# Kernel optimization log

Hardware: AMD Instinct MI355X
Metric: run time of the kernel (lower is better)

## Reference

```python
import jax, jax.numpy as jnp
import numpy as np

N = 200_000   # nodes in batched graph
E = 6_400_000 # edges
G = 1024      # graphs in the batch
H = 256       # hidden_dim


def setup_inputs() -> dict:
    key = jax.random.key(0)
    ks = jax.random.split(key, 20)
    src = jax.random.randint(ks[0], (E,), 0, N, dtype=jnp.int32)
    dst = jax.random.randint(ks[1], (E,), 0, N, dtype=jnp.int32)
    graph_ids = jnp.sort(jax.random.randint(ks[2], (N,), 0, G, dtype=jnp.int32))

    def lin(k, fi, fo):
        kw, kb = jax.random.split(k)
        s = 1.0 / np.sqrt(fi)
        return (jax.random.normal(kw, (fi, fo), jnp.float32) * s,
                jax.random.normal(kb, (fo,), jnp.float32) * s)

    W1, b1 = lin(ks[3], 4, H)
    W2, b2 = lin(ks[4], H, H)
    W3, b3 = lin(ks[5], H, H)
    W4, b4 = lin(ks[6], H, H)
    W5, b5 = lin(ks[7], H, H)
    Wl1, bl1 = lin(ks[8], H, H // 2)
    Wl2, bl2 = lin(ks[9], H // 2, 1)
    return dict(src=src, dst=dst, graph_ids=graph_ids,
                W1=W1, b1=b1, W2=W2, b2=b2, W3=W3, b3=b3, W4=W4, b4=b4,
                W5=W5, b5=b5, Wl1=Wl1, bl1=bl1, Wl2=Wl2, bl2=bl2)


def reference(src, dst, graph_ids, W1, b1, W2, b2, W3, b3, W4, b4, W5, b5,
              Wl1, bl1, Wl2, bl2):
    ones_e = jnp.ones((E,), jnp.float32)
    deg_in = jax.ops.segment_sum(ones_e, dst, num_segments=N)   # in_degrees
    deg_out = jax.ops.segment_sum(ones_e, src, num_segments=N)  # out_degrees

    # node features from in-degrees (as in the torch forward)
    h1 = deg_in
    h2 = (deg_in - 3.0 > 0).astype(jnp.float32)
    h3 = 3.0 / h1
    h4 = (deg_in - 4.0 > 0).astype(jnp.float32)
    h_ = jnp.stack([h1, h2, h3, h4], axis=1)  # [N,4]

    # DGL GraphConv norm='both': D_out^{-1/2} on src side, D_in^{-1/2} on dst side
    norm_src = jax.lax.rsqrt(jnp.clip(deg_out, 1.0))[:, None]  # [N,1]
    norm_dst = jax.lax.rsqrt(jnp.clip(deg_in, 1.0))[:, None]

    def gconv(x, W, b):
        xs = x * norm_src
        agg = jax.ops.segment_sum(xs[src], dst, num_segments=N)  # SpMM
        return (agg * norm_dst) @ W + b

    h = jnp.tanh(gconv(h_, W1, b1))
    h = jnp.tanh(gconv(h, W2, b2))
    h = jnp.tanh(gconv(h, W3, b3))
    h = jnp.tanh(gconv(h, W4, b4))
    h = jnp.tanh(gconv(h, W5, b5))  # [N,H]

    # dgl.mean_nodes: per-graph mean over nodes
    gsum = jax.ops.segment_sum(h, graph_ids, num_segments=G)           # [G,H]
    cnt = jax.ops.segment_sum(jnp.ones((N,), jnp.float32), graph_ids,
                              num_segments=G)[:, None]
    graph_emb = jnp.where(cnt > 0, gsum / jnp.clip(cnt, 1.0), 0.0)

    h_emb = jax.nn.leaky_relu(graph_emb @ Wl1 + bl1, negative_slope=0.01)
    # dropout is identity in eval mode
    pred = jax.nn.sigmoid(h_emb @ Wl2 + bl2)
    return pred, graph_emb, h
```

## Files before the change

kernel.cpp:

```cpp
#include <hip/hip_runtime.h>
#include <hip/hip_fp16.h>

#define NN 200000
#define EE 6400000
#define GG 1024
#define HH 256
#define RR 8
#define NB 782
#define NC 782
#define CHUNK 8192
#define CAP 9216

typedef _Float16 half8 __attribute__((ext_vector_type(8)));
typedef float floatx4 __attribute__((ext_vector_type(4)));
typedef unsigned int uintx2 __attribute__((ext_vector_type(2)));

__device__ __forceinline__ float fast_tanh(float x) {
  float e = __expf(2.0f * x);
  return 1.0f - 2.0f / (e + 1.0f);
}

__global__ void degree_src_kernel(const int* __restrict__ src, int* __restrict__ doutR) {
  int e = blockIdx.x * blockDim.x + threadIdx.x;
  if (e >= EE) return;
  atomicAdd(&doutR[(e & (RR - 1)) * NN + src[e]], 1);
}

__global__ void gptr_kernel(const int* __restrict__ gid, int* __restrict__ g_ptr) {
  int n = blockIdx.x * blockDim.x + threadIdx.x;
  if (n >= NN) return;
  int g = gid[n];
  int gp = (n == 0) ? -1 : gid[n - 1];
  for (int x = gp + 1; x <= g; ++x) g_ptr[x] = n;
  if (n == NN - 1) {
    for (int x = g + 1; x <= GG; ++x) g_ptr[x] = NN;
  }
}

__global__ __launch_bounds__(256) void hist1_kernel(const int* __restrict__ dst,
                                                    int* __restrict__ hist_t) {
  __shared__ int h[NB];
  int c = blockIdx.x, t = threadIdx.x;
  for (int b = t; b < NB; b += 256) h[b] = 0;
  __syncthreads();
  int e0 = c * CHUNK, e1 = min(e0 + CHUNK, EE);
  for (int e = e0 + t; e < e1; e += 256) atomicAdd(&h[dst[e] >> 8], 1);
  __syncthreads();
  for (int b = t; b < NB; b += 256) hist_t[b * NC + c] = h[b];
}

__global__ __launch_bounds__(256) void scanA4_kernel(int* __restrict__ a, int n,
                                                     int* __restrict__ bsum) {
  __shared__ int ws4[4];
  int t = threadIdx.x;
  int base = blockIdx.x * 1024 + t * 4;
  int v0 = 0, v1 = 0, v2 = 0, v3 = 0;
  if (base + 3 < n) {
    int4 q = *(const int4*)(a + base);
    v0 = q.x; v1 = q.y; v2 = q.z; v3 = q.w;
  } else {
    if (base + 0 < n) v0 = a[base + 0];
    if (base + 1 < n) v1 = a[base + 1];
    if (base + 2 < n) v2 = a[base + 2];
    if (base + 3 < n) v3 = a[base + 3];
  }
  int s = v0 + v1 + v2 + v3;
  int lane = t & 63, w = t >> 6;
  int x = s;
  for (int off = 1; off < 64; off <<= 1) {
    int y = __shfl_up(x, off);
    if (lane >= off) x += y;
  }
  if (lane == 63) ws4[w] = x;
  __syncthreads();
  if (t == 0) {
    int acc = 0;
    for (int k = 0; k < 4; ++k) { int tmp = ws4[k]; ws4[k] = acc; acc += tmp; }
  }
  __syncthreads();
  int e = ws4[w] + x - s;
  int o0 = e, o1 = e + v0, o2 = o1 + v1, o3 = o2 + v2;
  if (base + 3 < n) {
    int4 q; q.x = o0; q.y = o1; q.z = o2; q.w = o3;
    *(int4*)(a + base) = q;
  } else {
    if (base + 0 < n) a[base + 0] = o0;
    if (base + 1 < n) a[base + 1] = o1;
    if (base + 2 < n) a[base + 2] = o2;
    if (base + 3 < n) a[base + 3] = o3;
  }
  if (t == 255) bsum[blockIdx.x] = ws4[3] + x;
}

__global__ __launch_bounds__(1024) void scanB_kernel(const int* __restrict__ bsum, int nb,
                                                     int* __restrict__ boffs) {
  __shared__ int wsum[16];
  int t = threadIdx.x;
  int lane = t & 63, w = t >> 6;
  int v = (t < nb) ? bsum[t] : 0;
  int x = v;
  for (int off = 1; off < 64; off <<= 1) {
    int y = __shfl_up(x, off);
    if (lane >= off) x += y;
  }
  if (lane == 63) wsum[w] = x;
  __syncthreads();
  if (t < 16) {
    int s = wsum[t];
    for (int off = 1; off < 16; off <<= 1) {
      int y = __shfl_up(s, off);
      if (t >= off) s += y;
    }
    wsum[t] = s;
  }
  __syncthreads();
  int waveoff = (w > 0) ? wsum[w - 1] : 0;
  int excl = waveoff + (x - v);
  if (t <= nb) boffs[t] = excl;
}

__global__ void addC4_kernel(int* __restrict__ a, int n, const int* __restrict__ boffs) {
  int i = blockIdx.x * blockDim.x + threadIdx.x;
  if (i < n) a[i] += boffs[i >> 10];
}

__global__ void bucketptr_kernel(const int* __restrict__ hist_t, int* __restrict__ bucket_ptr) {
  int b = blockIdx.x * blockDim.x + threadIdx.x;
  if (b < NB) bucket_ptr[b] = hist_t[b * NC];
  if (b == NB) bucket_ptr[NB] = EE;
}

__global__ __launch_bounds__(256) void scatter1_kernel(const int* __restrict__ src,
                                                       const int* __restrict__ dst,
                                                       const int* __restrict__ hist_t,
                                                       uint2* __restrict__ pairs) {
  __shared__ int cur[NB];
  int c = blockIdx.x, t = threadIdx.x;
  for (int b = t; b < NB; b += 256) cur[b] = hist_t[b * NC + c];
  __syncthreads();
  int e0 = c * CHUNK, e1 = min(e0 + CHUNK, EE);
  for (int e = e0 + t; e < e1; e += 256) {
    int d = dst[e], s = src[e];
    int pos = atomicAdd(&cur[d >> 8], 1);
    uint2 p; p.x = (unsigned)d; p.y = (unsigned)s;
    pairs[pos] = p;
  }
}

__global__ __launch_bounds__(256) void bucket_kernel(const uint2* __restrict__ pairs,
                                                     const int* __restrict__ bucket_ptr,
                                                     int* __restrict__ col,
                                                     int* __restrict__ row_ptr) {
  __shared__ int rhist[256];
  __shared__ int rcur[256];
  __shared__ int ws4[4];
  __shared__ int stage[CAP];
  int b = blockIdx.x, t = threadIdx.x;
  int row0 = b << 8;
  int p0 = bucket_ptr[b], p1 = bucket_ptr[b + 1];
  int cnt = p1 - p0;
  rhist[t] = 0;
  __syncthreads();
  for (int i = t; i < cnt; i += 256) {
    int d = (int)pairs[p0 + i].x;
    atomicAdd(&rhist[d & 255], 1);
  }
  __syncthreads();
  int v = rhist[t];
  int lane = t & 63, w = t >> 6;
  int x = v;
  for (int off = 1; off < 64; off <<= 1) {
    int y = __shfl_up(x, off);
    if (lane >= off) x += y;
  }
  if (lane == 63) ws4[w] = x;
  __syncthreads();
  if (t == 0) {
    int acc = 0;
    for (int k = 0; k < 4; ++k) { int tmp = ws4[k]; ws4[k] = acc; acc += tmp; }
  }
  __syncthreads();
  int excl = ws4[w] + x - v;
  rcur[t] = excl;
  int row = row0 + t;
  if (row < NN) row_ptr[row] = p0 + excl;
  if (b == NB - 1 && t == 0) row_ptr[NN] = EE;
  __syncthreads();
  for (int i = t; i < cnt; i += 256) {
    uint2 p = pairs[p0 + i];
    int pos = atomicAdd(&rcur[(int)p.x & 255], 1);
    if (pos < CAP) stage[pos] = (int)p.y;
    else col[p0 + pos] = (int)p.y;
  }
  __syncthreads();
  int lim = min(cnt, CAP);
  for (int i = t; i < lim; i += 256) col[p0 + i] = stage[i];
}

__global__ void feature_kernel(const int* __restrict__ row_ptr, const int* __restrict__ doutR,
                               float* __restrict__ norm_src, float* __restrict__ norm_dst,
                               float4* __restrict__ xs1) {
  int n = blockIdx.x * blockDim.x + threadIdx.x;
  if (n >= NN) return;
  int dii = row_ptr[n + 1] - row_ptr[n];
  int doo = 0;
#pragma unroll
  for (int r = 0; r < RR; ++r) doo += doutR[r * NN + n];
  float di = (float)dii;
  float dofl = (float)doo;
  float ns = rsqrtf(fmaxf(dofl, 1.0f));
  float nd = rsqrtf(fmaxf(di, 1.0f));
  norm_src[n] = ns;
  norm_dst[n] = nd;
  float h1 = di;
  float h2 = (di - 3.0f > 0.0f) ? 1.0f : 0.0f;
  float h3 = 3.0f / di;
  float h4 = (di - 4.0f > 0.0f) ? 1.0f : 0.0f;
  float4 o;
  o.x = h1 * ns; o.y = h2 * ns; o.z = h3 * ns; o.w = h4 * ns;
  xs1[n] = o;
}

__global__ void spmm4_kernel(const int* __restrict__ rp, const int* __restrict__ col,
                             const float4* __restrict__ xs1, const float* __restrict__ norm_dst,
                             float4* __restrict__ agg4) {
  int n = blockIdx.x * blockDim.x + threadIdx.x;
  if (n >= NN) return;
  int e0 = rp[n], e1 = rp[n + 1];
  float ax = 0.f, ay = 0.f, az = 0.f, aw = 0.f;
  for (int e = e0; e < e1; ++e) {
    int s = __builtin_nontemporal_load(&col[e]);
    float4 v = xs1[s];
    ax += v.x; ay += v.y; az += v.z; aw += v.w;
  }
  float nd = norm_dst[n];
  float4 o; o.x = ax * nd; o.y = ay * nd; o.z = az * nd; o.w = aw * nd;
  agg4[n] = o;
}

__device__ __forceinline__ void acc_row(uint2 v, float& a0, float& a1, float& a2, float& a3) {
  __half2 h0 = *reinterpret_cast<__half2*>(&v.x);
  __half2 h1 = *reinterpret_cast<__half2*>(&v.y);
  float2 f0 = __half22float2(h0);
  float2 f1 = __half22float2(h1);
  a0 += f0.x; a1 += f0.y; a2 += f1.x; a3 += f1.y;
}

__global__ __launch_bounds__(256) void spmm256_kernel(
    const int* __restrict__ rp, const int* __restrict__ col,
    const __half* __restrict__ hs, const float* __restrict__ norm_dst,
    __half* __restrict__ aggH) {
  int wid = (blockIdx.x * blockDim.x + threadIdx.x) >> 6;
  int lane = threadIdx.x & 63;
  if (wid >= NN) return;
  int e0 = rp[wid], e1 = rp[wid + 1];
  float a0 = 0.f, a1 = 0.f, a2 = 0.f, a3 = 0.f;
  const __half* hp = hs + lane * 4;
  int e = e0;
  for (; e + 16 <= e1; e += 16) {
    int s[16];
#pragma unroll
    for (int u = 0; u < 16; ++u)
      s[u] = __builtin_amdgcn_readfirstlane(__builtin_nontemporal_load(&col[e + u]));
    uint2 v[16];
#pragma unroll
    for (int u = 0; u < 16; ++u) v[u] = *(const uint2*)(hp + (size_t)s[u] * HH);
#pragma unroll
    for (int u = 0; u < 16; ++u) acc_row(v[u], a0, a1, a2, a3);
  }
  for (; e + 4 <= e1; e += 4) {
    int s[4];
#pragma unroll
    for (int u = 0; u < 4; ++u)
      s[u] = __builtin_amdgcn_readfirstlane(__builtin_nontemporal_load(&col[e + u]));
    uint2 v[4];
#pragma unroll
    for (int u = 0; u < 4; ++u) v[u] = *(const uint2*)(hp + (size_t)s[u] * HH);
#pragma unroll
    for (int u = 0; u < 4; ++u) acc_row(v[u], a0, a1, a2, a3);
  }
  for (; e < e1; ++e) {
    int s = __builtin_amdgcn_readfirstlane(__builtin_nontemporal_load(&col[e]));
    uint2 v = *(const uint2*)(hp + (size_t)s * HH);
    acc_row(v, a0, a1, a2, a3);
  }
  float nd = norm_dst[wid];
  __half2 p0 = __floats2half2_rn(a0 * nd, a1 * nd);
  __half2 p1 = __floats2half2_rn(a2 * nd, a3 * nd);
  uintx2 o;
  o[0] = *(unsigned*)&p0;
  o[1] = *(unsigned*)&p1;
  __builtin_nontemporal_store(o, (uintx2*)(aggH + (size_t)wid * HH + lane * 4));
}

__global__ __launch_bounds__(256) void transform4_kernel(
    const float* __restrict__ agg, const float* __restrict__ W, const float* __restrict__ b,
    const float* __restrict__ norm_src, __half* __restrict__ hs_out) {
  __shared__ float tile[64 * 4];
  int t = threadIdx.x;
  int rowbase = blockIdx.x * 64;
  const float4* srcp = (const float4*)(agg + (size_t)rowbase * 4);
  float4* dst4 = (float4*)tile;
  for (int i = t; i < 64; i += 256) dst4[i] = srcp[i];
  __syncthreads();
  int w = t >> 6, lane = t & 63;
  int c0 = lane * 4;
  float acc[16][4];
#pragma unroll
  for (int r = 0; r < 16; ++r) {
    acc[r][0] = 0.f; acc[r][1] = 0.f; acc[r][2] = 0.f; acc[r][3] = 0.f;
  }
  const float* tw = tile + (size_t)(w * 16) * 4;
#pragma unroll
  for (int k = 0; k < 4; ++k) {
    float4 wv = *(const float4*)(W + (size_t)k * HH + c0);
#pragma unroll
    for (int r = 0; r < 16; ++r) {
      float a = tw[r * 4 + k];
      acc[r][0] += a * wv.x;
      acc[r][1] += a * wv.y;
      acc[r][2] += a * wv.z;
      acc[r][3] += a * wv.w;
    }
  }
  float4 bv = *(const float4*)(b + c0);
#pragma unroll
  for (int r = 0; r < 16; ++r) {
    int row = rowbase + w * 16 + r;
    float ns = norm_src[row];
    float y0 = fast_tanh(acc[r][0] + bv.x) * ns;
    float y1 = fast_tanh(acc[r][1] + bv.y) * ns;
    float y2 = fast_tanh(acc[r][2] + bv.z) * ns;
    float y3 = fast_tanh(acc[r][3] + bv.w) * ns;
    __half2 p0 = __floats2half2_rn(y0, y1);
    __half2 p1 = __floats2half2_rn(y2, y3);
    uint2 o = make_uint2(*(unsigned*)&p0, *(unsigned*)&p1);
    *(uint2*)(hs_out + (size_t)row * HH + c0) = o;
  }
}

__global__ void repack_w_kernel(const float* __restrict__ W2, const float* __restrict__ W3,
                                const float* __restrict__ W4, const float* __restrict__ W5,
                                __half* __restrict__ Wf) {
  int t = blockIdx.x * blockDim.x + threadIdx.x;
  int which = t >> 16;
  int u = t & 65535;
  const float* W = (which == 0) ? W2 : (which == 1) ? W3 : (which == 2) ? W4 : W5;
  int b = u & 7;
  int lane = (u >> 3) & 63;
  int tile = (u >> 9) & 15;
  int ks = u >> 13;
  int k = ks * 32 + (lane >> 4) * 8 + b;
  int c = tile * 16 + (lane & 15);
  Wf[t] = __float2half(W[k * HH + c]);
}

__global__ __launch_bounds__(256) void gemm_mfma_kernel(
    const __half* __restrict__ aggH, const __half* __restrict__ Wf,
    const float* __restrict__ bias, const float* __restrict__ norm_src,
    __half* __restrict__ hs_out, float* h_out) {
  int w = threadIdx.x >> 6;
  int lane = threadIdx.x & 63;
  int l15 = lane & 15, l4 = lane >> 4;
  int row0 = blockIdx.x * 64;
  floatx4 acc[4][4];
#pragma unroll
  for (int m = 0; m < 4; ++m)
#pragma unroll
    for (int n = 0; n < 4; ++n) acc[m][n] = (floatx4)(0.0f);

#pragma unroll
  for (int ks = 0; ks < 8; ++ks) {
    int k0 = ks * 32 + l4 * 8;
    half8 af[4];
#pragma unroll
    for (int m = 0; m < 4; ++m)
      af[m] = *(const half8*)(aggH + (size_t)(row0 + m * 16 + l15) * HH + k0);
    half8 bf[4];
#pragma unroll
    for (int n = 0; n < 4; ++n)
      bf[n] = *(const half8*)(Wf + ((size_t)(ks * 16 + w * 4 + n) * 64 + lane) * 8);
#pragma unroll
    for (int m = 0; m < 4; ++m)
#pragma unroll
      for (int n = 0; n < 4; ++n)
        acc[m][n] = __builtin_amdgcn_mfma_f32_16x16x32_f16(af[m], bf[n], acc[m][n], 0, 0, 0);
  }

  float ns[16];
  if (!h_out) {
#pragma unroll
    for (int m = 0; m < 4; ++m)
#pragma unroll
      for (int r = 0; r < 4; ++r) ns[m * 4 + r] = norm_src[row0 + m * 16 + l4 * 4 + r];
  }
#pragma unroll
  for (int n = 0; n < 4; ++n) {
    int c = w * 64 + n * 16 + l15;
    float bb = bias[c];
#pragma unroll
    for (int m = 0; m < 4; ++m) {
#pragma unroll
      for (int r = 0; r < 4; ++r) {
        int row = row0 + m * 16 + l4 * 4 + r;
        float y = fast_tanh(acc[m][n][r] + bb);
        if (h_out) {
          h_out[(size_t)row * HH + c] = y;
        } else {
          hs_out[(size_t)row * HH + c] = (__half)(y * ns[m * 4 + r]);
        }
      }
    }
  }
}

__global__ void mean_kernel(const float* __restrict__ h, const int* __restrict__ g_ptr,
                            float* __restrict__ emb) {
  int g = blockIdx.x;
  int j = threadIdx.x;
  int s = g_ptr[g], e = g_ptr[g + 1];
  float sum = 0.f;
  for (int n = s; n < e; ++n) sum += h[(size_t)n * HH + j];
  int cnt = e - s;
  emb[(size_t)g * HH + j] = (cnt > 0) ? sum / (float)cnt : 0.0f;
}

__global__ __launch_bounds__(128) void mlp_kernel(const float* __restrict__ emb,
                                                  const float* __restrict__ Wl1,
                                                  const float* __restrict__ bl1,
                                                  const float* __restrict__ Wl2,
                                                  const float* __restrict__ bl2,
                                                  float* __restrict__ pred) {
  __shared__ float se[256];
  __shared__ float sh[128];
  int g = blockIdx.x, t = threadIdx.x;
  se[t] = emb[(size_t)g * HH + t];
  se[t + 128] = emb[(size_t)g * HH + t + 128];
  __syncthreads();
  float acc = bl1[t];
  for (int k = 0; k < 256; ++k) acc += se[k] * Wl1[k * 128 + t];
  float he = (acc > 0.f) ? acc : 0.01f * acc;
  sh[t] = he * Wl2[t];
  __syncthreads();
  if (t < 64) sh[t] += sh[t + 64];
  __syncthreads();
  if (t < 64) {
    float v = sh[t];
    for (int off = 32; off > 0; off >>= 1) v += __shfl_down(v, off);
    if (t == 0) {
      float z = v + bl2[0];
      pred[g] = 1.0f / (1.0f + expf(-z));
    }
  }
}

extern "C" void kernel_launch(void* const* d_in, const int* in_sizes, int n_in,
                              void* d_out, int out_size, void* d_ws, size_t ws_size,
                              hipStream_t stream) {
  const int* src = (const int*)d_in[0];
  const int* dst = (const int*)d_in[1];
  const int* gid = (const int*)d_in[2];
  const float* W1 = (const float*)d_in[3];
  const float* b1 = (const float*)d_in[4];
  const float* W2 = (const float*)d_in[5];
  const float* b2 = (const float*)d_in[6];
  const float* W3 = (const float*)d_in[7];
  const float* b3 = (const float*)d_in[8];
  const float* W4 = (const float*)d_in[9];
  const float* b4 = (const float*)d_in[10];
  const float* W5 = (const float*)d_in[11];
  const float* b5 = (const float*)d_in[12];
  const float* Wl1 = (const float*)d_in[13];
  const float* bl1 = (const float*)d_in[14];
  const float* Wl2 = (const float*)d_in[15];
  const float* bl2 = (const float*)d_in[16];

  char* ws = (char*)d_ws;
  size_t off = 0;
  auto alloc = [&](size_t bytes) -> void* {
    void* p = ws + off;
    off += (bytes + 255) & ~(size_t)255;
    return p;
  };

  int* col = (int*)alloc((size_t)EE * 4);
  int* row_ptr = (int*)alloc((size_t)(NN + 1) * 4);
  int* hist_t = (int*)alloc((size_t)NB * NC * 4);
  int* bucket_ptr = (int*)alloc((size_t)(NB + 1) * 4);
  int* bsum = (int*)alloc(1024 * 4);
  int* boffs = (int*)alloc(1025 * 4);
  int* g_ptr = (int*)alloc((size_t)(GG + 1) * 4);
  float* norm_src = (float*)alloc((size_t)NN * 4);
  float* norm_dst = (float*)alloc((size_t)NN * 4);
  float4* xs1 = (float4*)alloc((size_t)NN * 16);
  float4* agg4 = (float4*)alloc((size_t)NN * 16);
  __half* Wf = (__half*)alloc((size_t)4 * HH * HH * 2);
  int* doutR = (int*)alloc((size_t)RR * NN * 4);
  void* unionp = alloc((size_t)NN * HH * 2);
  uint2* pairs = (uint2*)unionp;
  __half* aggH = (__half*)unionp;

  float* outp = (float*)d_out;
  float* pred = outp;
  float* emb = outp + GG;
  float* hreg = outp + GG + (size_t)GG * HH;
  __half* hs = (__half*)hreg;

  hipMemsetAsync(doutR, 0, (size_t)RR * NN * 4, stream);

  degree_src_kernel<<<(EE + 255) / 256, 256, 0, stream>>>(src, doutR);
  gptr_kernel<<<(NN + 255) / 256, 256, 0, stream>>>(gid, g_ptr);
  repack_w_kernel<<<1024, 256, 0, stream>>>(W2, W3, W4, W5, Wf);

  const int nscan = NB * NC;
  const int nbA = (nscan + 1023) / 1024;
  hist1_kernel<<<NC, 256, 0, stream>>>(dst, hist_t);
  scanA4_kernel<<<nbA, 256, 0, stream>>>(hist_t, nscan, bsum);
  scanB_kernel<<<1, 1024, 0, stream>>>(bsum, nbA, boffs);
  addC4_kernel<<<(nscan + 255) / 256, 256, 0, stream>>>(hist_t, nscan, boffs);
  bucketptr_kernel<<<(NB + 256) / 256, 256, 0, stream>>>(hist_t, bucket_ptr);
  scatter1_kernel<<<NC, 256, 0, stream>>>(src, dst, hist_t, pairs);
  bucket_kernel<<<NB, 256, 0, stream>>>(pairs, bucket_ptr, col, row_ptr);

  feature_kernel<<<(NN + 255) / 256, 256, 0, stream>>>(row_ptr, doutR, norm_src, norm_dst, xs1);

  spmm4_kernel<<<(NN + 255) / 256, 256, 0, stream>>>(row_ptr, col, xs1, norm_dst, agg4);
  transform4_kernel<<<NN / 64, 256, 0, stream>>>((const float*)agg4, W1, b1, norm_src, hs);

  const float* bs[4] = {b2, b3, b4, b5};
  for (int l = 0; l < 4; ++l) {
    spmm256_kernel<<<NN / 4, 256, 0, stream>>>(row_ptr, col, hs, norm_dst, aggH);
    gemm_mfma_kernel<<<NN / 64, 256, 0, stream>>>(
        aggH, Wf + (size_t)l * HH * HH, bs[l], norm_src,
        hs, (l == 3) ? hreg : (float*)nullptr);
  }

  mean_kernel<<<GG, 256, 0, stream>>>(hreg, g_ptr, emb);
  mlp_kernel<<<GG, 128, 0, stream>>>(emb, Wl1, bl1, Wl2, bl2, pred);
}
```

Before: 2.961 ms.

## Split 256-wide SpMM into two 128-column passes for cache locality

Replaces the single SpMM over all 256 fp16 feature columns with two launches that each gather and accumulate one 128-column half. The intent is to shrink the randomly gathered working set per pass so more of it stays cache-resident. In exchange the column index and row pointer arrays are read twice, and each lane issues narrower 4-byte loads instead of 8-byte loads.

Measured after the change: 3.013 ms. Within noise of the previous version (+1.8%).

```diff
diff --git a/kernel.cpp b/kernel.cpp
--- a/kernel.cpp
+++ b/kernel.cpp
@@ -13,7 +13,6 @@
 
 typedef _Float16 half8 __attribute__((ext_vector_type(8)));
 typedef float floatx4 __attribute__((ext_vector_type(4)));
-typedef unsigned int uintx2 __attribute__((ext_vector_type(2)));
 
 __device__ __forceinline__ float fast_tanh(float x) {
   float e = __expf(2.0f * x);
@@ -238,59 +237,54 @@
   agg4[n] = o;
 }
 
-__device__ __forceinline__ void acc_row(uint2 v, float& a0, float& a1, float& a2, float& a3) {
-  __half2 h0 = *reinterpret_cast<__half2*>(&v.x);
-  __half2 h1 = *reinterpret_cast<__half2*>(&v.y);
-  float2 f0 = __half22float2(h0);
-  float2 f1 = __half22float2(h1);
-  a0 += f0.x; a1 += f0.y; a2 += f1.x; a3 += f1.y;
-}
-
-__global__ __launch_bounds__(256) void spmm256_kernel(
+__device__ __forceinline__ void acc_half2(unsigned v, float& a0, float& a1) {
+  __half2 h = *reinterpret_cast<__half2*>(&v);
+  float2 f = __half22float2(h);
+  a0 += f.x; a1 += f.y;
+}
+
+__global__ __launch_bounds__(256) void spmm128_kernel(
     const int* __restrict__ rp, const int* __restrict__ col,
     const __half* __restrict__ hs, const float* __restrict__ norm_dst,
-    __half* __restrict__ aggH) {
+    __half* __restrict__ aggH, int half) {
   int wid = (blockIdx.x * blockDim.x + threadIdx.x) >> 6;
   int lane = threadIdx.x & 63;
   if (wid >= NN) return;
   int e0 = rp[wid], e1 = rp[wid + 1];
-  float a0 = 0.f, a1 = 0.f, a2 = 0.f, a3 = 0.f;
-  const __half* hp = hs + lane * 4;
+  float a0 = 0.f, a1 = 0.f;
+  const __half* hp = hs + half * 128 + lane * 2;
   int e = e0;
   for (; e + 16 <= e1; e += 16) {
     int s[16];
 #pragma unroll
     for (int u = 0; u < 16; ++u)
       s[u] = __builtin_amdgcn_readfirstlane(__builtin_nontemporal_load(&col[e + u]));
-    uint2 v[16];
-#pragma unroll
-    for (int u = 0; u < 16; ++u) v[u] = *(const uint2*)(hp + (size_t)s[u] * HH);
-#pragma unroll
-    for (int u = 0; u < 16; ++u) acc_row(v[u], a0, a1, a2, a3);
+    unsigned v[16];
+#pragma unroll
+    for (int u = 0; u < 16; ++u) v[u] = *(const unsigned*)(hp + (size_t)s[u] * HH);
+#pragma unroll
+    for (int u = 0; u < 16; ++u) acc_half2(v[u], a0, a1);
   }
   for (; e + 4 <= e1; e += 4) {
     int s[4];
 #pragma unroll
     for (int u = 0; u < 4; ++u)
       s[u] = __builtin_amdgcn_readfirstlane(__builtin_nontemporal_load(&col[e + u]));
-    uint2 v[4];
-#pragma unroll
-    for (int u = 0; u < 4; ++u) v[u] = *(const uint2*)(hp + (size_t)s[u] * HH);
-#pragma unroll
-    for (int u = 0; u < 4; ++u) acc_row(v[u], a0, a1, a2, a3);
+    unsigned v[4];
+#pragma unroll
+    for (int u = 0; u < 4; ++u) v[u] = *(const unsigned*)(hp + (size_t)s[u] * HH);
+#pragma unroll
+    for (int u = 0; u < 4; ++u) acc_half2(v[u], a0, a1);
   }
   for (; e < e1; ++e) {
     int s = __builtin_amdgcn_readfirstlane(__builtin_nontemporal_load(&col[e]));
-    uint2 v = *(const uint2*)(hp + (size_t)s * HH);
-    acc_row(v, a0, a1, a2, a3);
+    unsigned v = *(const unsigned*)(hp + (size_t)s * HH);
+    acc_half2(v, a0, a1);
   }
   float nd = norm_dst[wid];
-  __half2 p0 = __floats2half2_rn(a0 * nd, a1 * nd);
-  __half2 p1 = __floats2half2_rn(a2 * nd, a3 * nd);
-  uintx2 o;
-  o[0] = *(unsigned*)&p0;
-  o[1] = *(unsigned*)&p1;
-  __builtin_nontemporal_store(o, (uintx2*)(aggH + (size_t)wid * HH + lane * 4));
+  __half2 p = __floats2half2_rn(a0 * nd, a1 * nd);
+  __builtin_nontemporal_store(*(unsigned*)&p,
+                              (unsigned*)(aggH + (size_t)wid * HH + half * 128 + lane * 2));
 }
 
 __global__ __launch_bounds__(256) void transform4_kernel(
@@ -529,7 +523,8 @@
 
   const float* bs[4] = {b2, b3, b4, b5};
   for (int l = 0; l < 4; ++l) {
-    spmm256_kernel<<<NN / 4, 256, 0, stream>>>(row_ptr, col, hs, norm_dst, aggH);
+    spmm128_kernel<<<NN / 4, 256, 0, stream>>>(row_ptr, col, hs, norm_dst, aggH, 0);
+    spmm128_kernel<<<NN / 4, 256, 0, stream>>>(row_ptr, col, hs, norm_dst, aggH, 1);
     gemm_mfma_kernel<<<NN / 64, 256, 0, stream>>>(
         aggH, Wf + (size_t)l * HH * HH, bs[l], norm_src,
         hs, (l == 3) ? hreg : (float*)nullptr);
```

## Fuse SpMM aggregation with MFMA GEMM and compute out-degree via bucket sort

Applied to the files above, without the earlier changes.

Replaces the separate spmm256 and gemm kernels for layers 2-4 with one fused kernel. It aggregates 64 rows into an LDS tile and runs the MFMA transform from there, so the fp16 aggregate buffer no longer makes a round trip through global memory. It also replaces the atomic global out-degree histogram (8 replicated counters plus a memset) with a radix-style scatter of src and a per-bucket shared-memory histogram. The trade-offs are lower occupancy, since each block serializes 16 rows per wave of gather before the GEMM, and extra scan and scatter passes for the degree computation.

After: 2.969 ms. No clear change (+0.3%).

```diff
diff --git a/kernel.cpp b/kernel.cpp
--- a/kernel.cpp
+++ b/kernel.cpp
@@ -5,11 +5,11 @@
 #define EE 6400000
 #define GG 1024
 #define HH 256
-#define RR 8
 #define NB 782
 #define NC 782
 #define CHUNK 8192
 #define CAP 9216
+#define LP 264
 
 typedef _Float16 half8 __attribute__((ext_vector_type(8)));
 typedef float floatx4 __attribute__((ext_vector_type(4)));
@@ -18,12 +18,6 @@
 __device__ __forceinline__ float fast_tanh(float x) {
   float e = __expf(2.0f * x);
   return 1.0f - 2.0f / (e + 1.0f);
-}
-
-__global__ void degree_src_kernel(const int* __restrict__ src, int* __restrict__ doutR) {
-  int e = blockIdx.x * blockDim.x + threadIdx.x;
-  if (e >= EE) return;
-  atomicAdd(&doutR[(e & (RR - 1)) * NN + src[e]], 1);
 }
 
 __global__ void gptr_kernel(const int* __restrict__ gid, int* __restrict__ g_ptr) {
@@ -37,14 +31,14 @@
   }
 }
 
-__global__ __launch_bounds__(256) void hist1_kernel(const int* __restrict__ dst,
+__global__ __launch_bounds__(256) void hist1_kernel(const int* __restrict__ key,
                                                     int* __restrict__ hist_t) {
   __shared__ int h[NB];
   int c = blockIdx.x, t = threadIdx.x;
   for (int b = t; b < NB; b += 256) h[b] = 0;
   __syncthreads();
   int e0 = c * CHUNK, e1 = min(e0 + CHUNK, EE);
-  for (int e = e0 + t; e < e1; e += 256) atomicAdd(&h[dst[e] >> 8], 1);
+  for (int e = e0 + t; e < e1; e += 256) atomicAdd(&h[key[e] >> 8], 1);
   __syncthreads();
   for (int b = t; b < NB; b += 256) hist_t[b * NC + c] = h[b];
 }
@@ -197,15 +191,43 @@
   for (int i = t; i < lim; i += 256) col[p0 + i] = stage[i];
 }
 
-__global__ void feature_kernel(const int* __restrict__ row_ptr, const int* __restrict__ doutR,
+__global__ __launch_bounds__(256) void scatter_src_kernel(const int* __restrict__ src,
+                                                          const int* __restrict__ hist_t,
+                                                          int* __restrict__ out) {
+  __shared__ int cur[NB];
+  int c = blockIdx.x, t = threadIdx.x;
+  for (int b = t; b < NB; b += 256) cur[b] = hist_t[b * NC + c];
+  __syncthreads();
+  int e0 = c * CHUNK, e1 = min(e0 + CHUNK, EE);
+  for (int e = e0 + t; e < e1; e += 256) {
+    int v = src[e];
+    int pos = atomicAdd(&cur[v >> 8], 1);
+    out[pos] = v;
+  }
+}
+
+__global__ __launch_bounds__(256) void buckethist_kernel(const int* __restrict__ sorted,
+                                                         const int* __restrict__ hist_t,
+                                                         int* __restrict__ deg_out) {
+  __shared__ int h[256];
+  int b = blockIdx.x, t = threadIdx.x;
+  int p0 = hist_t[b * NC];
+  int p1 = (b == NB - 1) ? EE : hist_t[(b + 1) * NC];
+  h[t] = 0;
+  __syncthreads();
+  for (int i = p0 + t; i < p1; i += 256) atomicAdd(&h[sorted[i] & 255], 1);
+  __syncthreads();
+  int n = (b << 8) + t;
+  if (n < NN) deg_out[n] = h[t];
+}
+
+__global__ void feature_kernel(const int* __restrict__ row_ptr, const int* __restrict__ deg_out,
                                float* __restrict__ norm_src, float* __restrict__ norm_dst,
                                float4* __restrict__ xs1) {
   int n = blockIdx.x * blockDim.x + threadIdx.x;
   if (n >= NN) return;
   int dii = row_ptr[n + 1] - row_ptr[n];
-  int doo = 0;
-#pragma unroll
-  for (int r = 0; r < RR; ++r) doo += doutR[r * NN + n];
+  int doo = deg_out[n];
   float di = (float)dii;
   float dofl = (float)doo;
   float ns = rsqrtf(fmaxf(dofl, 1.0f));
@@ -291,6 +313,93 @@
   o[0] = *(unsigned*)&p0;
   o[1] = *(unsigned*)&p1;
   __builtin_nontemporal_store(o, (uintx2*)(aggH + (size_t)wid * HH + lane * 4));
+}
+
+__global__ __launch_bounds__(256, 4) void fused_kernel(
+    const int* __restrict__ rp, const int* __restrict__ col,
+    const __half* __restrict__ hs, const float* __restrict__ norm_dst,
+    const __half* __restrict__ Wf, const float* __restrict__ bias,
+    const float* __restrict__ norm_src, __half* __restrict__ hs_out) {
+  __shared__ __half tileA[64 * LP];
+  int t = threadIdx.x;
+  int w = t >> 6, lane = t & 63;
+  int row0 = blockIdx.x * 64;
+  const __half* hp = hs + lane * 4;
+
+  for (int r = 0; r < 16; ++r) {
+    int row = row0 + w * 16 + r;
+    int e0 = rp[row], e1 = rp[row + 1];
+    float a0 = 0.f, a1 = 0.f, a2 = 0.f, a3 = 0.f;
+    int e = e0;
+    for (; e + 8 <= e1; e += 8) {
+      int s[8];
+#pragma unroll
+      for (int u = 0; u < 8; ++u)
+        s[u] = __builtin_amdgcn_readfirstlane(__builtin_nontemporal_load(&col[e + u]));
+      uint2 v[8];
+#pragma unroll
+      for (int u = 0; u < 8; ++u) v[u] = *(const uint2*)(hp + (size_t)s[u] * HH);
+#pragma unroll
+      for (int u = 0; u < 8; ++u) acc_row(v[u], a0, a1, a2, a3);
+    }
+    for (; e < e1; ++e) {
+      int s = __builtin_amdgcn_readfirstlane(__builtin_nontemporal_load(&col[e]));
+      uint2 v = *(const uint2*)(hp + (size_t)s * HH);
+      acc_row(v, a0, a1, a2, a3);
+    }
+    float nd = norm_dst[row];
+    __half2 p0 = __floats2half2_rn(a0 * nd, a1 * nd);
+    __half2 p1 = __floats2half2_rn(a2 * nd, a3 * nd);
+    unsigned* dst = (unsigned*)(tileA + (w * 16 + r) * LP + lane * 4);
+    dst[0] = *(unsigned*)&p0;
+    dst[1] = *(unsigned*)&p1;
+  }
+  __syncthreads();
+
+  int l15 = lane & 15, l4 = lane >> 4;
+  floatx4 acc[4][4];
+#pragma unroll
+  for (int m = 0; m < 4; ++m)
+#pragma unroll
+    for (int n = 0; n < 4; ++n) acc[m][n] = (floatx4)(0.0f);
+
+#pragma unroll
+  for (int ks = 0; ks < 8; ++ks) {
+    int k0 = ks * 32 + l4 * 8;
+    half8 af[4];
+#pragma unroll
+    for (int m = 0; m < 4; ++m)
+      af[m] = *(const half8*)(tileA + (m * 16 + l15) * LP + k0);
+    half8 bf[4];
+#pragma unroll
+    for (int n = 0; n < 4; ++n)
+      bf[n] = *(const half8*)(Wf + ((size_t)(ks * 16 + w * 4 + n) * 64 + lane) * 8);
+#pragma unroll
+    for (int m = 0; m < 4; ++m)
+#pragma unroll
+      for (int n = 0; n < 4; ++n)
+        acc[m][n] = __builtin_amdgcn_mfma_f32_16x16x32_f16(af[m], bf[n], acc[m][n], 0, 0, 0);
+  }
+
+  float ns[16];
+#pragma unroll
+  for (int m = 0; m < 4; ++m)
+#pragma unroll
+    for (int r = 0; r < 4; ++r) ns[m * 4 + r] = norm_src[row0 + m * 16 + l4 * 4 + r];
+#pragma unroll
+  for (int n = 0; n < 4; ++n) {
+    int c = w * 64 + n * 16 + l15;
+    float bb = bias[c];
+#pragma unroll
+    for (int m = 0; m < 4; ++m) {
+#pragma unroll
+      for (int r = 0; r < 4; ++r) {
+        int row = row0 + m * 16 + l4 * 4 + r;
+        float y = fast_tanh(acc[m][n][r] + bb);
+        hs_out[(size_t)row * HH + c] = (__half)(y * ns[m * 4 + r]);
+      }
+    }
+  }
 }
 
 __global__ __launch_bounds__(256) void transform4_kernel(
@@ -357,8 +466,7 @@
 
 __global__ __launch_bounds__(256) void gemm_mfma_kernel(
     const __half* __restrict__ aggH, const __half* __restrict__ Wf,
-    const float* __restrict__ bias, const float* __restrict__ norm_src,
-    __half* __restrict__ hs_out, float* h_out) {
+    const float* __restrict__ bias, float* __restrict__ h_out) {
   int w = threadIdx.x >> 6;
   int lane = threadIdx.x & 63;
   int l15 = lane & 15, l4 = lane >> 4;
@@ -387,13 +495,6 @@
         acc[m][n] = __builtin_amdgcn_mfma_f32_16x16x32_f16(af[m], bf[n], acc[m][n], 0, 0, 0);
   }
 
-  float ns[16];
-  if (!h_out) {
-#pragma unroll
-    for (int m = 0; m < 4; ++m)
-#pragma unroll
-      for (int r = 0; r < 4; ++r) ns[m * 4 + r] = norm_src[row0 + m * 16 + l4 * 4 + r];
-  }
 #pragma unroll
   for (int n = 0; n < 4; ++n) {
     int c = w * 64 + n * 16 + l15;
@@ -403,12 +504,7 @@
 #pragma unroll
       for (int r = 0; r < 4; ++r) {
         int row = row0 + m * 16 + l4 * 4 + r;
-        float y = fast_tanh(acc[m][n][r] + bb);
-        if (h_out) {
-          h_out[(size_t)row * HH + c] = y;
-        } else {
-          hs_out[(size_t)row * HH + c] = (__half)(y * ns[m * 4 + r]);
-        }
+        h_out[(size_t)row * HH + c] = fast_tanh(acc[m][n][r] + bb);
       }
     }
   }
@@ -490,25 +586,24 @@
   int* bsum = (int*)alloc(1024 * 4);
   int* boffs = (int*)alloc(1025 * 4);
   int* g_ptr = (int*)alloc((size_t)(GG + 1) * 4);
+  int* deg_out = (int*)alloc((size_t)NN * 4);
   float* norm_src = (float*)alloc((size_t)NN * 4);
   float* norm_dst = (float*)alloc((size_t)NN * 4);
   float4* xs1 = (float4*)alloc((size_t)NN * 16);
   float4* agg4 = (float4*)alloc((size_t)NN * 16);
   __half* Wf = (__half*)alloc((size_t)4 * HH * HH * 2);
-  int* doutR = (int*)alloc((size_t)RR * NN * 4);
   void* unionp = alloc((size_t)NN * HH * 2);
   uint2* pairs = (uint2*)unionp;
+  int* src_sorted = (int*)unionp;
+  __half* hsA = (__half*)unionp;
   __half* aggH = (__half*)unionp;
 
   float* outp = (float*)d_out;
   float* pred = outp;
   float* emb = outp + GG;
   float* hreg = outp + GG + (size_t)GG * HH;
-  __half* hs = (__half*)hreg;
-
-  hipMemsetAsync(doutR, 0, (size_t)RR * NN * 4, stream);
-
-  degree_src_kernel<<<(EE + 255) / 256, 256, 0, stream>>>(src, doutR);
+  __half* hsB = (__half*)hreg;
+
   gptr_kernel<<<(NN + 255) / 256, 256, 0, stream>>>(gid, g_ptr);
   repack_w_kernel<<<1024, 256, 0, stream>>>(W2, W3, W4, W5, Wf);
 
@@ -522,18 +617,27 @@
   scatter1_kernel<<<NC, 256, 0, stream>>>(src, dst, hist_t, pairs);
   bucket_kernel<<<NB, 256, 0, stream>>>(pairs, bucket_ptr, col, row_ptr);
 
-  feature_kernel<<<(NN + 255) / 256, 256, 0, stream>>>(row_ptr, doutR, norm_src, norm_dst, xs1);
+  hist1_kernel<<<NC, 256, 0, stream>>>(src, hist_t);
+  scanA4_kernel<<<nbA, 256, 0, stream>>>(hist_t, nscan, bsum);
+  scanB_kernel<<<1, 1024, 0, stream>>>(bsum, nbA, boffs);
+  addC4_kernel<<<(nscan + 255) / 256, 256, 0, stream>>>(hist_t, nscan, boffs);
+  scatter_src_kernel<<<NC, 256, 0, stream>>>(src, hist_t, src_sorted);
+  buckethist_kernel<<<NB, 256, 0, stream>>>(src_sorted, hist_t, deg_out);
+
+  feature_kernel<<<(NN + 255) / 256, 256, 0, stream>>>(row_ptr, deg_out, norm_src, norm_dst, xs1);
 
   spmm4_kernel<<<(NN + 255) / 256, 256, 0, stream>>>(row_ptr, col, xs1, norm_dst, agg4);
-  transform4_kernel<<<NN / 64, 256, 0, stream>>>((const float*)agg4, W1, b1, norm_src, hs);
-
-  const float* bs[4] = {b2, b3, b4, b5};
-  for (int l = 0; l < 4; ++l) {
-    spmm256_kernel<<<NN / 4, 256, 0, stream>>>(row_ptr, col, hs, norm_dst, aggH);
-    gemm_mfma_kernel<<<NN / 64, 256, 0, stream>>>(
-        aggH, Wf + (size_t)l * HH * HH, bs[l], norm_src,
-        hs, (l == 3) ? hreg : (float*)nullptr);
-  }
+  transform4_kernel<<<NN / 64, 256, 0, stream>>>((const float*)agg4, W1, b1, norm_src, hsA);
+
+  fused_kernel<<<NN / 64, 256, 0, stream>>>(row_ptr, col, hsA, norm_dst,
+                                            Wf + 0 * HH * HH, b2, norm_src, hsB);
+  fused_kernel<<<NN / 64, 256, 0, stream>>>(row_ptr, col, hsB, norm_dst,
+                                            Wf + 1 * (size_t)HH * HH, b3, norm_src, hsA);
+  fused_kernel<<<NN / 64, 256, 0, stream>>>(row_ptr, col, hsA, norm_dst,
+                                            Wf + 2 * (size_t)HH * HH, b4, norm_src, hsB);
+
+  spmm256_kernel<<<NN / 4, 256, 0, stream>>>(row_ptr, col, hsB, norm_dst, aggH);
+  gemm_mfma_kernel<<<NN / 64, 256, 0, stream>>>(aggH, Wf + 3 * (size_t)HH * HH, b5, hreg);
 
   mean_kernel<<<GG, 256, 0, stream>>>(hreg, g_ptr, emb);
   mlp_kernel<<<GG, 128, 0, stream>>>(emb, Wl1, bl1, Wl2, bl2, pred);
```

## Replace global-atomic out-degree with bucket-sort histogram and pack CSR sort keys

Applied to the files above, without the earlier changes.

Out-degree counting moves off global atomics over a replicated array and onto a bucketed counting sort of src. That sort uses a shared-memory histogram fused into the dst histogram pass, a second scan, a scatter, and per-bucket LDS counting. The dst-sort intermediate shrinks from 8-byte (dst,src) pairs to 4-byte keys that pack the low dst bits with src, halving scatter and bucket traffic. The change adds extra scan and scatter passes over the 6.4M edges and a second histogram buffer, and relies on src fitting in 24 bits.

New measurement: 2.831 ms. 4.4% less time.

```diff
diff --git a/kernel.cpp b/kernel.cpp
--- a/kernel.cpp
+++ b/kernel.cpp
@@ -5,7 +5,6 @@
 #define EE 6400000
 #define GG 1024
 #define HH 256
-#define RR 8
 #define NB 782
 #define NC 782
 #define CHUNK 8192
@@ -18,12 +17,6 @@
 __device__ __forceinline__ float fast_tanh(float x) {
   float e = __expf(2.0f * x);
   return 1.0f - 2.0f / (e + 1.0f);
-}
-
-__global__ void degree_src_kernel(const int* __restrict__ src, int* __restrict__ doutR) {
-  int e = blockIdx.x * blockDim.x + threadIdx.x;
-  if (e >= EE) return;
-  atomicAdd(&doutR[(e & (RR - 1)) * NN + src[e]], 1);
 }
 
 __global__ void gptr_kernel(const int* __restrict__ gid, int* __restrict__ g_ptr) {
@@ -37,16 +30,25 @@
   }
 }
 
-__global__ __launch_bounds__(256) void hist1_kernel(const int* __restrict__ dst,
-                                                    int* __restrict__ hist_t) {
-  __shared__ int h[NB];
+__global__ __launch_bounds__(256) void hist_dual_kernel(const int* __restrict__ dst,
+                                                        const int* __restrict__ src,
+                                                        int* __restrict__ hist_d,
+                                                        int* __restrict__ hist_s) {
+  __shared__ int hd[NB];
+  __shared__ int hsb[NB];
   int c = blockIdx.x, t = threadIdx.x;
-  for (int b = t; b < NB; b += 256) h[b] = 0;
+  for (int b = t; b < NB; b += 256) { hd[b] = 0; hsb[b] = 0; }
   __syncthreads();
   int e0 = c * CHUNK, e1 = min(e0 + CHUNK, EE);
-  for (int e = e0 + t; e < e1; e += 256) atomicAdd(&h[dst[e] >> 8], 1);
-  __syncthreads();
-  for (int b = t; b < NB; b += 256) hist_t[b * NC + c] = h[b];
+  for (int e = e0 + t; e < e1; e += 256) {
+    atomicAdd(&hd[dst[e] >> 8], 1);
+    atomicAdd(&hsb[src[e] >> 8], 1);
+  }
+  __syncthreads();
+  for (int b = t; b < NB; b += 256) {
+    hist_d[b * NC + c] = hd[b];
+    hist_s[b * NC + c] = hsb[b];
+  }
 }
 
 __global__ __launch_bounds__(256) void scanA4_kernel(int* __restrict__ a, int n,
@@ -124,31 +126,24 @@
   if (i < n) a[i] += boffs[i >> 10];
 }
 
-__global__ void bucketptr_kernel(const int* __restrict__ hist_t, int* __restrict__ bucket_ptr) {
-  int b = blockIdx.x * blockDim.x + threadIdx.x;
-  if (b < NB) bucket_ptr[b] = hist_t[b * NC];
-  if (b == NB) bucket_ptr[NB] = EE;
-}
-
 __global__ __launch_bounds__(256) void scatter1_kernel(const int* __restrict__ src,
                                                        const int* __restrict__ dst,
-                                                       const int* __restrict__ hist_t,
-                                                       uint2* __restrict__ pairs) {
+                                                       const int* __restrict__ hist_d,
+                                                       unsigned* __restrict__ keys) {
   __shared__ int cur[NB];
   int c = blockIdx.x, t = threadIdx.x;
-  for (int b = t; b < NB; b += 256) cur[b] = hist_t[b * NC + c];
+  for (int b = t; b < NB; b += 256) cur[b] = hist_d[b * NC + c];
   __syncthreads();
   int e0 = c * CHUNK, e1 = min(e0 + CHUNK, EE);
   for (int e = e0 + t; e < e1; e += 256) {
     int d = dst[e], s = src[e];
     int pos = atomicAdd(&cur[d >> 8], 1);
-    uint2 p; p.x = (unsigned)d; p.y = (unsigned)s;
-    pairs[pos] = p;
-  }
-}
-
-__global__ __launch_bounds__(256) void bucket_kernel(const uint2* __restrict__ pairs,
-                                                     const int* __restrict__ bucket_ptr,
+    keys[pos] = ((unsigned)(d & 255) << 24) | (unsigned)s;
+  }
+}
+
+__global__ __launch_bounds__(256) void bucket_kernel(const unsigned* __restrict__ keys,
+                                                     const int* __restrict__ hist_d,
                                                      int* __restrict__ col,
                                                      int* __restrict__ row_ptr) {
   __shared__ int rhist[256];
@@ -157,13 +152,13 @@
   __shared__ int stage[CAP];
   int b = blockIdx.x, t = threadIdx.x;
   int row0 = b << 8;
-  int p0 = bucket_ptr[b], p1 = bucket_ptr[b + 1];
+  int p0 = hist_d[b * NC];
+  int p1 = (b == NB - 1) ? EE : hist_d[(b + 1) * NC];
   int cnt = p1 - p0;
   rhist[t] = 0;
   __syncthreads();
   for (int i = t; i < cnt; i += 256) {
-    int d = (int)pairs[p0 + i].x;
-    atomicAdd(&rhist[d & 255], 1);
+    atomicAdd(&rhist[keys[p0 + i] >> 24], 1);
   }
   __syncthreads();
   int v = rhist[t];
@@ -187,25 +182,54 @@
   if (b == NB - 1 && t == 0) row_ptr[NN] = EE;
   __syncthreads();
   for (int i = t; i < cnt; i += 256) {
-    uint2 p = pairs[p0 + i];
-    int pos = atomicAdd(&rcur[(int)p.x & 255], 1);
-    if (pos < CAP) stage[pos] = (int)p.y;
-    else col[p0 + pos] = (int)p.y;
+    unsigned k = keys[p0 + i];
+    int pos = atomicAdd(&rcur[k >> 24], 1);
+    int s = (int)(k & 0xFFFFFFu);
+    if (pos < CAP) stage[pos] = s;
+    else col[p0 + pos] = s;
   }
   __syncthreads();
   int lim = min(cnt, CAP);
   for (int i = t; i < lim; i += 256) col[p0 + i] = stage[i];
 }
 
-__global__ void feature_kernel(const int* __restrict__ row_ptr, const int* __restrict__ doutR,
+__global__ __launch_bounds__(256) void scatter_src_kernel(const int* __restrict__ src,
+                                                          const int* __restrict__ hist_s,
+                                                          int* __restrict__ out) {
+  __shared__ int cur[NB];
+  int c = blockIdx.x, t = threadIdx.x;
+  for (int b = t; b < NB; b += 256) cur[b] = hist_s[b * NC + c];
+  __syncthreads();
+  int e0 = c * CHUNK, e1 = min(e0 + CHUNK, EE);
+  for (int e = e0 + t; e < e1; e += 256) {
+    int v = src[e];
+    int pos = atomicAdd(&cur[v >> 8], 1);
+    out[pos] = v;
+  }
+}
+
+__global__ __launch_bounds__(256) void buckethist_kernel(const int* __restrict__ sorted,
+                                                         const int* __restrict__ hist_s,
+                                                         int* __restrict__ deg_out) {
+  __shared__ int h[256];
+  int b = blockIdx.x, t = threadIdx.x;
+  int p0 = hist_s[b * NC];
+  int p1 = (b == NB - 1) ? EE : hist_s[(b + 1) * NC];
+  h[t] = 0;
+  __syncthreads();
+  for (int i = p0 + t; i < p1; i += 256) atomicAdd(&h[sorted[i] & 255], 1);
+  __syncthreads();
+  int n = (b << 8) + t;
+  if (n < NN) deg_out[n] = h[t];
+}
+
+__global__ void feature_kernel(const int* __restrict__ row_ptr, const int* __restrict__ deg_out,
                                float* __restrict__ norm_src, float* __restrict__ norm_dst,
                                float4* __restrict__ xs1) {
   int n = blockIdx.x * blockDim.x + threadIdx.x;
   if (n >= NN) return;
   int dii = row_ptr[n + 1] - row_ptr[n];
-  int doo = 0;
-#pragma unroll
-  for (int r = 0; r < RR; ++r) doo += doutR[r * NN + n];
+  int doo = deg_out[n];
   float di = (float)dii;
   float dofl = (float)doo;
   float ns = rsqrtf(fmaxf(dofl, 1.0f));
@@ -485,19 +509,20 @@
 
   int* col = (int*)alloc((size_t)EE * 4);
   int* row_ptr = (int*)alloc((size_t)(NN + 1) * 4);
-  int* hist_t = (int*)alloc((size_t)NB * NC * 4);
-  int* bucket_ptr = (int*)alloc((size_t)(NB + 1) * 4);
+  int* hist_d = (int*)alloc((size_t)NB * NC * 4);
+  int* hist_s = (int*)alloc((size_t)NB * NC * 4);
   int* bsum = (int*)alloc(1024 * 4);
   int* boffs = (int*)alloc(1025 * 4);
   int* g_ptr = (int*)alloc((size_t)(GG + 1) * 4);
+  int* deg_out = (int*)alloc((size_t)NN * 4);
   float* norm_src = (float*)alloc((size_t)NN * 4);
   float* norm_dst = (float*)alloc((size_t)NN * 4);
   float4* xs1 = (float4*)alloc((size_t)NN * 16);
   float4* agg4 = (float4*)alloc((size_t)NN * 16);
   __half* Wf = (__half*)alloc((size_t)4 * HH * HH * 2);
-  int* doutR = (int*)alloc((size_t)RR * NN * 4);
   void* unionp = alloc((size_t)NN * HH * 2);
-  uint2* pairs = (uint2*)unionp;
+  unsigned* keys = (unsigned*)unionp;
+  int* src_sorted = (int*)unionp;
   __half* aggH = (__half*)unionp;
 
   float* outp = (float*)d_out;
@@ -506,23 +531,24 @@
   float* hreg = outp + GG + (size_t)GG * HH;
   __half* hs = (__half*)hreg;
 
-  hipMemsetAsync(doutR, 0, (size_t)RR * NN * 4, stream);
-
-  degree_src_kernel<<<(EE + 255) / 256, 256, 0, stream>>>(src, doutR);
   gptr_kernel<<<(NN + 255) / 256, 256, 0, stream>>>(gid, g_ptr);
   repack_w_kernel<<<1024, 256, 0, stream>>>(W2, W3, W4, W5, Wf);
 
   const int nscan = NB * NC;
   const int nbA = (nscan + 1023) / 1024;
-  hist1_kernel<<<NC, 256, 0, stream>>>(dst, hist_t);
-  scanA4_kernel<<<nbA, 256, 0, stream>>>(hist_t, nscan, bsum);
+  hist_dual_kernel<<<NC, 256, 0, stream>>>(dst, src, hist_d, hist_s);
+  scanA4_kernel<<<nbA, 256, 0, stream>>>(hist_d, nscan, bsum);
   scanB_kernel<<<1, 1024, 0, stream>>>(bsum, nbA, boffs);
-  addC4_kernel<<<(nscan + 255) / 256, 256, 0, stream>>>(hist_t, nscan, boffs);
-  bucketptr_kernel<<<(NB + 256) / 256, 256, 0, stream>>>(hist_t, bucket_ptr);
-  scatter1_kernel<<<NC, 256, 0, stream>>>(src, dst, hist_t, pairs);
-  bucket_kernel<<<NB, 256, 0, stream>>>(pairs, bucket_ptr, col, row_ptr);
-
-  feature_kernel<<<(NN + 255) / 256, 256, 0, stream>>>(row_ptr, doutR, norm_src, norm_dst, xs1);
+  addC4_kernel<<<(nscan + 255) / 256, 256, 0, stream>>>(hist_d, nscan, boffs);
+  scatter1_kernel<<<NC, 256, 0, stream>>>(src, dst, hist_d, keys);
+  bucket_kernel<<<NB, 256, 0, stream>>>(keys, hist_d, col, row_ptr);
+  scanA4_kernel<<<nbA, 256, 0, stream>>>(hist_s, nscan, bsum);
+  scanB_kernel<<<1, 1024, 0, stream>>>(bsum, nbA, boffs);
+  addC4_kernel<<<(nscan + 255) / 256, 256, 0, stream>>>(hist_s, nscan, boffs);
+  scatter_src_kernel<<<NC, 256, 0, stream>>>(src, hist_s, src_sorted);
+  buckethist_kernel<<<NB, 256, 0, stream>>>(src_sorted, hist_s, deg_out);
+
+  feature_kernel<<<(NN + 255) / 256, 256, 0, stream>>>(row_ptr, deg_out, norm_src, norm_dst, xs1);
 
   spmm4_kernel<<<(NN + 255) / 256, 256, 0, stream>>>(row_ptr, col, xs1, norm_dst, agg4);
   transform4_kernel<<<NN / 64, 256, 0, stream>>>((const float*)agg4, W1, b1, norm_src, hs);
```
